# Performance work log

Measured on AMD Instinct MI355X. Metric: run time of the kernel, lower is better.

The kernel has to match this reference:

```python
import jax, jax.numpy as jnp
import numpy as np

N_QUBITS = 12
N_LAYERS = 6
BATCH = 512
DIM = 2 ** N_QUBITS


def _apply_1q(psi, G, wire):
    """Apply a single-qubit gate on `wire` (wire 0 = most significant).
    psi: [B, 2^n] complex. G: [2,2] (shared) or [B,2,2] (batched)."""
    B = psi.shape[0]
    left = 2 ** wire
    psi = psi.reshape(B, left, 2, -1)
    if G.ndim == 2:
        psi = jnp.einsum('ij,bxjy->bxiy', G, psi)
    else:
        psi = jnp.einsum('bij,bxjy->bxiy', G, psi)
    return psi.reshape(B, -1)


def _apply_cnot(psi, c, t):
    """CNOT with control c, target t on [B, 2^n] state."""
    B = psi.shape[0]
    ps = psi.reshape((B,) + (2,) * N_QUBITS)
    ca, ta = c + 1, t + 1
    c0 = jnp.take(ps, 0, axis=ca)
    c1 = jnp.take(ps, 1, axis=ca)
    flip_ax = ta if ta < ca else ta - 1
    c1 = jnp.flip(c1, axis=flip_ax)  # X on target within control=1 block
    ps = jnp.stack([c0, c1], axis=ca)
    return ps.reshape(B, -1)


def _circuit(x, weights):
    B = x.shape[0]
    psi = jnp.zeros((B, DIM), jnp.complex64).at[:, 0].set(1.0)

    # AngleEmbedding: RY(x_w) on each wire (batched gate matrices)
    h = 0.5 * x
    c, s = jnp.cos(h).astype(jnp.complex64), jnp.sin(h).astype(jnp.complex64)
    for w in range(N_QUBITS):
        G = jnp.stack([jnp.stack([c[:, w], -s[:, w]], -1),
                       jnp.stack([s[:, w], c[:, w]], -1)], -2)  # [B,2,2]
        psi = _apply_1q(psi, G, w)

    # StronglyEntanglingLayers: Rot(phi,theta,omega) per wire, then ring of CNOTs
    for l in range(N_LAYERS):
        phi, theta, omega = weights[l, :, 0], weights[l, :, 1], weights[l, :, 2]
        ct = jnp.cos(0.5 * theta).astype(jnp.complex64)
        st = jnp.sin(0.5 * theta).astype(jnp.complex64)
        ep = jnp.exp(-0.5j * (phi + omega).astype(jnp.complex64))
        em = jnp.exp(0.5j * (phi - omega).astype(jnp.complex64))
        # Rot = RZ(omega) RY(theta) RZ(phi)
        m00 = ep * ct
        m01 = -em * st
        m10 = jnp.conj(em) * st
        m11 = jnp.conj(ep) * ct
        for w in range(N_QUBITS):
            G = jnp.array([[m00[w], m01[w]], [m10[w], m11[w]]], jnp.complex64)
            psi = _apply_1q(psi, G, w)
        r = l % (N_QUBITS - 1) + 1
        for w in range(N_QUBITS):
            psi = _apply_cnot(psi, w, (w + r) % N_QUBITS)

    # <Z_w> for every wire
    probs = psi.real ** 2 + psi.imag ** 2  # [B, 2^n]
    exps = []
    for w in range(N_QUBITS):
        p = probs.reshape(B, 2 ** w, 2, -1)
        exps.append(p[:, :, 0, :].sum((1, 2)) - p[:, :, 1, :].sum((1, 2)))
    return jnp.stack(exps, -1)  # [B, n_qubits]


def setup_inputs() -> dict:
    key = jax.random.key(0)
    k1, k2, k3, k4 = jax.random.split(key, 4)
    x = jax.random.uniform(k1, (BATCH, N_QUBITS), jnp.float32, -np.pi, np.pi)
    weights = jax.random.uniform(k2, (N_LAYERS, N_QUBITS, 3), jnp.float32, 0.0, 2.0 * np.pi)
    W = jax.random.normal(k3, (1, N_QUBITS), jnp.float32) * 0.3
    b = jax.random.normal(k4, (1,), jnp.float32) * 0.01
    return {"x": x, "weights": weights, "W": W, "b": b}


def reference(x, weights, W, b):
    z = _circuit(x, weights)              # [B, n_qubits]
    y = z @ W.T + b                       # [B, 1]
    return y.squeeze(-1)                  # [B]
```

## Files before the change

kernel.cpp:

```cpp
#include <hip/hip_runtime.h>
#include <stdint.h>

#define NQ 12
#define DIM 4096
#define NLAYERS 6
#define TPB 256

typedef float v2f __attribute__((ext_vector_type(2)));

struct Pass_t {
    uint32_t WT[8];
    uint32_t WL[8];
    uint32_t RT[8];
    uint32_t RL[16];
    bool r64;
};
struct Pass10_t {
    uint32_t WT[6];
    uint32_t WL[8];
    uint32_t RT[6];
    uint32_t RL[16];
    bool r64;
};
struct CK_t {
    Pass10_t PS1, PS2;
    Pass_t PS3;
    Pass_t P1[NLAYERS];
    uint32_t frow[NQ];
};

constexpr uint32_t S1f(uint32_t k){ return ((k&7u)<<3) | ((k>>3)&7u) | (k & 0xFC0u); }
constexpr uint32_t S2f(uint32_t k){ return ((k&7u)<<6) | (k & 0x38u) | ((k>>6)&7u) | (k & 0xE00u); }
constexpr uint32_t S3f(uint32_t k){ return ((k&7u)<<9) | (k & 0x1F8u) | ((k>>9)&7u); }

constexpr uint32_t ech_reduce(const uint32_t* v, int n, uint32_t x){
    bool ch = true;
    while (ch) {
        ch = false;
        for (int i = 0; i < n; i++)
            if (v[i] && (x ^ v[i]) < x) { x ^= v[i]; ch = true; }
    }
    return x;
}

constexpr Pass_t build_pass(const uint32_t* Mc) {
    Pass_t P{};
    bool r64 = (Mc[3] == 8u);
    for (int j = 0; j < 12; j++) if (j != 3 && (Mc[j] & 8u)) r64 = false;
    P.r64 = r64;
    uint32_t rows[12]{};
    rows[0] = 8u;
    int nr = 1;
    uint32_t full[12]{}; int nf = 0; full[nf++] = 8u;
    uint32_t We[4]{};  int nw = 0;
    uint32_t Re[5]{};  int nre = 0;
    const int rpn = r64 ? 4 : 5;
    if (!r64) {
        uint32_t p0 = 0;
        for (int j = 0; j < rpn; j++)
            p0 |= (uint32_t)(__builtin_popcount(8u & Mc[4 + j]) & 1) << j;
        uint32_t r = ech_reduce(Re, nre, p0);
        if (r) Re[nre++] = r;
    }
    for (int slot = 0; slot < 4; slot++) {
        uint32_t chosen = 0;
        for (int relax = 0; relax < 3 && !chosen; relax++) {
            for (uint32_t m = 1; m < 4096u && !chosen; m++) {
                if (m & 8u) continue;
                uint32_t wp = (m >> 4) & 15u;
                uint32_t wr = ech_reduce(We, nw, wp);
                if (relax < 2 && !wr) continue;
                uint32_t rp = 0;
                for (int j = 0; j < rpn; j++)
                    rp |= (uint32_t)(__builtin_popcount(m & Mc[4 + j]) & 1) << j;
                uint32_t rr = ech_reduce(Re, nre, rp);
                if (relax < 1 && !rr) continue;
                uint32_t fr = ech_reduce(full, nf, m);
                if (!fr) continue;
                chosen = m; full[nf++] = fr;
                if (wr && nw < 4) We[nw++] = wr;
                if (rr && nre < 5) Re[nre++] = rr;
            }
        }
        rows[nr++] = chosen;
    }
    for (int slot = nr; slot < 12; slot++) {
        for (uint32_t m = 1; m < 4096u; m++) {
            if (m & 8u) continue;
            uint32_t fr = ech_reduce(full, nf, m);
            if (fr) { rows[slot] = m; full[nf++] = fr; break; }
        }
    }
    uint32_t col[12]{}, lmc[12]{};
    for (int j = 0; j < 12; j++) {
        uint32_t c = 0;
        for (int i = 0; i < 12; i++) c |= (uint32_t)((rows[i] >> j) & 1u) << i;
        col[j] = c;
    }
    for (int j = 0; j < 12; j++) {
        uint32_t a = 0, mc = Mc[j];
        for (int q = 0; q < 12; q++) if ((mc >> q) & 1u) a ^= col[q];
        lmc[j] = a;
    }
    for (int j = 0; j < 8; j++) { P.WT[j] = col[4 + j]; P.RT[j] = lmc[4 + j]; }
    for (int j = 0; j < 8; j++) {
        uint32_t a = 0;
        for (int q = 0; q < 3; q++) if ((j >> q) & 1) a ^= col[q];
        P.WL[j] = a;
    }
    for (int l = 0; l < 16; l++) {
        uint32_t a = 0;
        for (int q = 0; q < 4; q++) if ((l >> q) & 1) a ^= lmc[q];
        P.RL[l] = a;
    }
    return P;
}

constexpr Pass10_t build_pass10(const uint32_t* Mc) {
    Pass10_t P{};
    bool r64 = (Mc[3] == 8u);
    for (int j = 0; j < 10; j++) if (j != 3 && (Mc[j] & 8u)) r64 = false;
    P.r64 = r64;
    uint32_t rows[10]{};
    rows[0] = 8u;
    int nr = 1;
    uint32_t full[10]{}; int nf = 0; full[nf++] = 8u;
    uint32_t We[4]{};  int nw = 0;
    uint32_t Re[5]{};  int nre = 0;
    const int rpn = r64 ? 4 : 5;
    if (!r64) {
        uint32_t p0 = 0;
        for (int j = 0; j < rpn; j++)
            p0 |= (uint32_t)(__builtin_popcount(8u & Mc[4 + j]) & 1) << j;
        uint32_t r = ech_reduce(Re, nre, p0);
        if (r) Re[nre++] = r;
    }
    for (int slot = 0; slot < 4; slot++) {
        uint32_t chosen = 0;
        for (int relax = 0; relax < 3 && !chosen; relax++) {
            for (uint32_t m = 1; m < 1024u && !chosen; m++) {
                if (m & 8u) continue;
                uint32_t wp = (m >> 4) & 15u;
                uint32_t wr = ech_reduce(We, nw, wp);
                if (relax < 2 && !wr) continue;
                uint32_t rp = 0;
                for (int j = 0; j < rpn; j++)
                    rp |= (uint32_t)(__builtin_popcount(m & Mc[4 + j]) & 1) << j;
                uint32_t rr = ech_reduce(Re, nre, rp);
                if (relax < 1 && !rr) continue;
                uint32_t fr = ech_reduce(full, nf, m);
                if (!fr) continue;
                chosen = m; full[nf++] = fr;
                if (wr && nw < 4) We[nw++] = wr;
                if (rr && nre < 5) Re[nre++] = rr;
            }
        }
        rows[nr++] = chosen;
    }
    for (int slot = nr; slot < 10; slot++) {
        for (uint32_t m = 1; m < 1024u; m++) {
            if (m & 8u) continue;
            uint32_t fr = ech_reduce(full, nf, m);
            if (fr) { rows[slot] = m; full[nf++] = fr; break; }
        }
    }
    uint32_t col[10]{}, lmc[10]{};
    for (int j = 0; j < 10; j++) {
        uint32_t c = 0;
        for (int i = 0; i < 10; i++) c |= (uint32_t)((rows[i] >> j) & 1u) << i;
        col[j] = c;
    }
    for (int j = 0; j < 10; j++) {
        uint32_t a = 0, mc = Mc[j];
        for (int q = 0; q < 10; q++) if ((mc >> q) & 1u) a ^= col[q];
        lmc[j] = a;
    }
    for (int j = 0; j < 6; j++) { P.WT[j] = col[4 + j]; P.RT[j] = lmc[4 + j]; }
    for (int j = 0; j < 8; j++) {
        uint32_t a = 0;
        for (int q = 0; q < 3; q++) if ((j >> q) & 1) a ^= col[q];
        P.WL[j] = a;
    }
    for (int l = 0; l < 16; l++) {
        uint32_t a = 0;
        for (int q = 0; q < 4; q++) if ((l >> q) & 1) a ^= lmc[q];
        P.RL[l] = a;
    }
    return P;
}

constexpr CK_t build_ck() {
    CK_t ck{};
    uint32_t Acols[NLAYERS][NQ]{}, Aicol5[NQ]{};
    for (int l = 0; l < NLAYERS; l++) {
        int r = l % (NQ - 1) + 1;
        for (int q = 0; q < NQ; q++) {
            uint32_t v = 1u << q;
            for (int w = NQ - 1; w >= 0; w--) {
                int pc = NQ - 1 - w, pt = NQ - 1 - ((w + r) % NQ);
                v ^= ((v >> pc) & 1u) << pt;
            }
            Acols[l][q] = v;
            if (l == NLAYERS - 1) {
                uint32_t u = 1u << q;
                for (int w = 0; w < NQ; w++) {
                    int pc = NQ - 1 - w, pt = NQ - 1 - ((w + r) % NQ);
                    u ^= ((u >> pc) & 1u) << pt;
                }
                Aicol5[q] = u;
            }
        }
    }
    uint32_t Mc10[10]{};
    for (int j = 0; j < 10; j++) Mc10[j] = S1f(1u << j);
    ck.PS1 = build_pass10(Mc10);
    for (int j = 0; j < 10; j++) Mc10[j] = S2f(1u << j);
    ck.PS2 = build_pass10(Mc10);
    uint32_t Mc[12]{};
    for (int j = 0; j < 12; j++) Mc[j] = S3f(1u << j);
    ck.PS3 = build_pass(Mc);
    for (int l = 1; l < NLAYERS; l++) {
        for (int j = 0; j < 12; j++) Mc[j] = S3f(S2f(S1f(Acols[l - 1][j])));
        ck.P1[l] = build_pass(Mc);
    }
    uint32_t Mcol[NQ]{};
    for (int j = 0; j < NQ; j++) {
        uint32_t pj = S1f(S2f(S3f(1u << j)));
        uint32_t M = 0;
        for (int m = 0; m < NQ; m++) if ((pj >> m) & 1u) M ^= Aicol5[m];
        Mcol[j] = M;
    }
    for (int p = 0; p < NQ; p++) {
        uint32_t s = 0;
        for (int j = 0; j < NQ; j++) s |= ((Mcol[j] >> p) & 1u) << j;
        ck.frow[p] = s;
    }
    return ck;
}
constexpr CK_t CK = build_ck();
static_assert(CK.PS2.r64, "S2 must fix the pack bit (b64 reads)");
static_assert(CK.PS3.r64, "S3 must fix the pack bit (b64 reads)");

template<int Q>
__device__ __forceinline__ void gate_q(v2f (&PRE)[8], v2f (&PIM)[8], float4 m) {
    v2f bx = {m.x, m.x}, by = {m.y, m.y}, bz = {m.z, m.z}, bw = {m.w, m.w};
    #pragma unroll
    for (int j = 0; j < 8; j++) {
        if (j & (1 << Q)) continue;
        int j2 = j | (1 << Q);
        v2f re0 = PRE[j], im0 = PIM[j], re1 = PRE[j2], im1 = PIM[j2];
        PRE[j]  = __builtin_elementwise_fma(bx, re0,
                  __builtin_elementwise_fma(by, -im0,
                  __builtin_elementwise_fma(bz, re1, -bw * im1)));
        PIM[j]  = __builtin_elementwise_fma(bx, im0,
                  __builtin_elementwise_fma(by, re0,
                  __builtin_elementwise_fma(bz, im1, bw * re1)));
        PRE[j2] = __builtin_elementwise_fma(bx, re1,
                  __builtin_elementwise_fma(by, im1,
                  __builtin_elementwise_fma(bz, -re0, -bw * im0)));
        PIM[j2] = __builtin_elementwise_fma(bx, im1,
                  __builtin_elementwise_fma(by, -re1,
                  __builtin_elementwise_fma(bz, -im0, bw * re0)));
    }
}

__device__ __forceinline__ void gate3(v2f (&PRE)[8], v2f (&PIM)[8],
                                      float4 g0, float4 g1, float4 g2) {
    gate_q<0>(PRE, PIM, g0);
    gate_q<1>(PRE, PIM, g1);
    gate_q<2>(PRE, PIM, g2);
}

__device__ __forceinline__ void s1_pass(v2f (&PRE)[8], v2f (&PIM)[8],
                                        float* buf, uint32_t wb, uint32_t rb) {
    constexpr Pass10_t P = CK.PS1;
    v2f* bre = (v2f*)buf;
    v2f* bim = (v2f*)(buf + DIM);
    #pragma unroll
    for (int j = 0; j < 8; j++) {
        uint32_t s = (wb ^ P.WL[j]) >> 1;
        bre[s] = PRE[j]; bim[s] = PIM[j];
    }
    __asm__ volatile("s_waitcnt lgkmcnt(0)" ::: "memory");
    #pragma unroll
    for (int j = 0; j < 8; j++) {
        uint32_t s0 = rb ^ P.RL[j], s1 = rb ^ P.RL[j | 8];
        v2f re, im;
        re.x = buf[s0];       re.y = buf[s1];
        im.x = buf[DIM + s0]; im.y = buf[DIM + s1];
        PRE[j] = re; PIM[j] = im;
    }
}

__device__ __forceinline__ void s2_pass(v2f (&PRE)[8], v2f (&PIM)[8],
                                        float* buf, uint32_t wb, uint32_t rb) {
    constexpr Pass10_t P = CK.PS2;
    v2f* bre = (v2f*)buf;
    v2f* bim = (v2f*)(buf + DIM);
    #pragma unroll
    for (int j = 0; j < 8; j++) {
        uint32_t s = (wb ^ P.WL[j]) >> 1;
        bre[s] = PRE[j]; bim[s] = PIM[j];
    }
    __asm__ volatile("s_waitcnt lgkmcnt(0)" ::: "memory");
    #pragma unroll
    for (int j = 0; j < 8; j++) {
        uint32_t s = (rb ^ P.RL[j]) >> 1;
        PRE[j] = bre[s]; PIM[j] = bim[s];
    }
}

__device__ __forceinline__ void s3_pass(v2f (&PRE)[8], v2f (&PIM)[8],
                                        float* buf, uint32_t wb, uint32_t rb) {
    constexpr Pass_t P = CK.PS3;
    v2f* bre = (v2f*)buf;
    v2f* bim = (v2f*)(buf + DIM);
    __syncthreads();
    #pragma unroll
    for (int j = 0; j < 8; j++) {
        uint32_t s = (wb ^ P.WL[j]) >> 1;
        bre[s] = PRE[j]; bim[s] = PIM[j];
    }
    __syncthreads();
    #pragma unroll
    for (int j = 0; j < 8; j++) {
        uint32_t s = (rb ^ P.RL[j]) >> 1;
        PRE[j] = bre[s]; PIM[j] = bim[s];
    }
}

__device__ __forceinline__ void rebase_pass(v2f (&PRE)[8], v2f (&PIM)[8],
                                            float* buf, int tid, int l) {
    const Pass_t& P = CK.P1[l];
    uint32_t wb = 0, rb = 0;
    #pragma unroll
    for (int j = 0; j < 8; j++) {
        uint32_t sel = (uint32_t)(-(int)((tid >> j) & 1));
        wb ^= sel & P.WT[j];
        rb ^= sel & P.RT[j];
    }
    v2f* bre = (v2f*)buf;
    v2f* bim = (v2f*)(buf + DIM);
    #pragma unroll
    for (int j = 0; j < 8; j++) {
        uint32_t s = (wb ^ P.WL[j]) >> 1;
        bre[s] = PRE[j]; bim[s] = PIM[j];
    }
    __syncthreads();
    #pragma unroll
    for (int j = 0; j < 8; j++) {
        uint32_t s0 = rb ^ P.RL[j], s1 = rb ^ P.RL[j | 8];
        v2f re, im;
        re.x = buf[s0];       re.y = buf[s1];
        im.x = buf[DIM + s0]; im.y = buf[DIM + s1];
        PRE[j] = re; PIM[j] = im;
    }
}

__global__ __launch_bounds__(TPB) void qsim_kernel(
    const float* __restrict__ x,
    const float* __restrict__ weights,
    const float* __restrict__ Wp,
    const float* __restrict__ bptr,
    float* __restrict__ out)
{
    __shared__ float  lds[2 * 2 * DIM];
    __shared__ float4 smat[NLAYERS * NQ];
    __shared__ float  scs[NQ], sss[NQ];
    __shared__ float  red[4];

    const int tid = threadIdx.x;
    const int b   = blockIdx.x;

    if (tid < NQ) {
        float s_, c_;
        sincosf(0.5f * x[b * NQ + tid], &s_, &c_);
        scs[tid] = c_; sss[tid] = s_;
    }
    if (tid < NLAYERS * NQ) {
        float phi   = weights[tid * 3 + 0];
        float theta = weights[tid * 3 + 1];
        float omega = weights[tid * 3 + 2];
        float st, ct; sincosf(0.5f * theta, &st, &ct);
        float sp, cp; sincosf(0.5f * (phi + omega), &sp, &cp);
        float sm, cm; sincosf(0.5f * (phi - omega), &sm, &cm);
        smat[tid] = make_float4(cp * ct, -sp * ct, -cm * st, -sm * st);
    }
    __syncthreads();

    float base = 1.0f;
    #pragma unroll
    for (int j = 0; j < 8; j++) {
        int w = 7 - j;
        base *= ((tid >> j) & 1) ? sss[w] : scs[w];
    }
    v2f PRE[8], PIM[8];
    float c8 = scs[8], s8 = sss[8];
    #pragma unroll
    for (int j = 0; j < 8; j++) {
        float a = base;
        #pragma unroll
        for (int p = 0; p < 3; p++) {
            int w = NQ - 1 - p;
            a *= ((j >> p) & 1) ? sss[w] : scs[w];
        }
        PRE[j].x = a * c8;  PRE[j].y = a * s8;
        PIM[j].x = 0.0f;    PIM[j].y = 0.0f;
    }

    uint32_t s1wb = 0, s1rb = 0, s2wb = 0, s2rb = 0, s3wb = 0, s3rb = 0;
    {
        constexpr Pass10_t Q1 = CK.PS1;
        constexpr Pass10_t Q2 = CK.PS2;
        constexpr Pass_t   Q3 = CK.PS3;
        #pragma unroll
        for (int j = 0; j < 6; j++) {
            uint32_t sel = (uint32_t)(-(int)((tid >> j) & 1));
            s1wb ^= sel & Q1.WT[j]; s1rb ^= sel & Q1.RT[j];
            s2wb ^= sel & Q2.WT[j]; s2rb ^= sel & Q2.RT[j];
        }
        #pragma unroll
        for (int j = 0; j < 8; j++) {
            uint32_t sel = (uint32_t)(-(int)((tid >> j) & 1));
            s3wb ^= sel & Q3.WT[j]; s3rb ^= sel & Q3.RT[j];
        }
        uint32_t wvb = (uint32_t)(tid & 0xC0) << 4;
        s1wb |= wvb; s1rb |= wvb; s2wb |= wvb; s2rb |= wvb;
    }

    float* bufA = lds;
    float* bufB = lds + 2 * DIM;

    #pragma clang loop unroll(disable)
    for (int l = 0; l < NLAYERS; l++) {
        if (l > 0) rebase_pass(PRE, PIM, bufB, tid, l);
        const int sb = l * NQ;
        gate3(PRE, PIM, smat[sb + 11], smat[sb + 10], smat[sb + 9]);
        s1_pass(PRE, PIM, bufA, s1wb, s1rb);
        gate3(PRE, PIM, smat[sb + 8], smat[sb + 7], smat[sb + 6]);
        s2_pass(PRE, PIM, bufA, s2wb, s2rb);
        gate3(PRE, PIM, smat[sb + 5], smat[sb + 4], smat[sb + 3]);
        s3_pass(PRE, PIM, bufA, s3wb, s3rb);
        gate3(PRE, PIM, smat[sb + 2], smat[sb + 1], smat[sb + 0]);
    }

    const float bv = bptr[0];
    float wbT[NQ];
    #pragma unroll
    for (int p = 0; p < NQ; p++) {
        uint32_t row = CK.frow[p];
        int tp = __popc(tid & (int)(row >> 4)) & 1;
        float Wv = Wp[NQ - 1 - p];
        wbT[p] = tp ? -Wv : Wv;
    }
    v2f acc2 = {0.0f, 0.0f};
    #pragma unroll
    for (int j = 0; j < 8; j++) {
        float cx = bv, cy = bv;
        #pragma unroll
        for (int p = 0; p < NQ; p++) {
            uint32_t row = CK.frow[p];
            float s = (__popc(j & (int)(row & 7u)) & 1) ? -wbT[p] : wbT[p];
            cx += s;
            cy += (row & 8u) ? -s : s;
        }
        v2f c = {cx, cy};
        acc2 += (PRE[j] * PRE[j] + PIM[j] * PIM[j]) * c;
    }
    float acc = acc2.x + acc2.y;
    #pragma unroll
    for (int off = 32; off > 0; off >>= 1)
        acc += __shfl_down(acc, off, 64);
    if ((tid & 63) == 0) red[tid >> 6] = acc;
    __syncthreads();
    if (tid == 0) out[b] = red[0] + red[1] + red[2] + red[3];
}

extern "C" void kernel_launch(void* const* d_in, const int* in_sizes, int n_in,
                              void* d_out, int out_size, void* d_ws, size_t ws_size,
                              hipStream_t stream) {
    const float* x       = (const float*)d_in[0];
    const float* weights = (const float*)d_in[1];
    const float* W       = (const float*)d_in[2];
    const float* bptr    = (const float*)d_in[3];
    qsim_kernel<<<512, TPB, 0, stream>>>(x, weights, W, bptr, (float*)d_out);
}
```

Before: 91.86 us.

## Apply gates on packed lane qubit to cut LDS exchange passes per layer

Each thread's state is held as 8 v2f pairs, with the second float of each pair treated as a fourth local qubit. A new pack_gate applies a gate directly on that packed bit using a lane swap. Gates are now grouped four per stage, so only two LDS permutation passes (PA, PB) run per layer instead of three. The PB pass now reads scalar floats rather than b64 pairs, because its layout no longer keeps the pack bit fixed. This adds extra VALU swizzle work and non-vectorized LDS reads.

```diff
diff --git a/kernel.cpp b/kernel.cpp
--- a/kernel.cpp
+++ b/kernel.cpp
@@ -13,25 +13,22 @@
     uint32_t WL[8];
     uint32_t RT[8];
     uint32_t RL[16];
-    bool r64;
 };
 struct Pass10_t {
     uint32_t WT[6];
     uint32_t WL[8];
     uint32_t RT[6];
     uint32_t RL[16];
-    bool r64;
 };
 struct CK_t {
-    Pass10_t PS1, PS2;
-    Pass_t PS3;
+    Pass10_t PA;
+    Pass_t PB;
     Pass_t P1[NLAYERS];
     uint32_t frow[NQ];
 };
 
-constexpr uint32_t S1f(uint32_t k){ return ((k&7u)<<3) | ((k>>3)&7u) | (k & 0xFC0u); }
-constexpr uint32_t S2f(uint32_t k){ return ((k&7u)<<6) | (k & 0x38u) | ((k>>6)&7u) | (k & 0xE00u); }
-constexpr uint32_t S3f(uint32_t k){ return ((k&7u)<<9) | (k & 0x1F8u) | ((k>>9)&7u); }
+constexpr uint32_t G2f(uint32_t k){ return ((k&15u)<<8) | (k&0xF0u) | ((k>>8)&15u); }
+constexpr uint32_t G3f(uint32_t k){ return ((k&15u)<<4) | ((k>>4)&15u) | (k&0xF00u); }
 
 constexpr uint32_t ech_reduce(const uint32_t* v, int n, uint32_t x){
     bool ch = true;
@@ -45,19 +42,15 @@
 
 constexpr Pass_t build_pass(const uint32_t* Mc) {
     Pass_t P{};
-    bool r64 = (Mc[3] == 8u);
-    for (int j = 0; j < 12; j++) if (j != 3 && (Mc[j] & 8u)) r64 = false;
-    P.r64 = r64;
     uint32_t rows[12]{};
     rows[0] = 8u;
     int nr = 1;
     uint32_t full[12]{}; int nf = 0; full[nf++] = 8u;
     uint32_t We[4]{};  int nw = 0;
     uint32_t Re[5]{};  int nre = 0;
-    const int rpn = r64 ? 4 : 5;
-    if (!r64) {
+    {
         uint32_t p0 = 0;
-        for (int j = 0; j < rpn; j++)
+        for (int j = 0; j < 5; j++)
             p0 |= (uint32_t)(__builtin_popcount(8u & Mc[4 + j]) & 1) << j;
         uint32_t r = ech_reduce(Re, nre, p0);
         if (r) Re[nre++] = r;
@@ -71,7 +64,7 @@
                 uint32_t wr = ech_reduce(We, nw, wp);
                 if (relax < 2 && !wr) continue;
                 uint32_t rp = 0;
-                for (int j = 0; j < rpn; j++)
+                for (int j = 0; j < 5; j++)
                     rp |= (uint32_t)(__builtin_popcount(m & Mc[4 + j]) & 1) << j;
                 uint32_t rr = ech_reduce(Re, nre, rp);
                 if (relax < 1 && !rr) continue;
@@ -118,19 +111,15 @@
 
 constexpr Pass10_t build_pass10(const uint32_t* Mc) {
     Pass10_t P{};
-    bool r64 = (Mc[3] == 8u);
-    for (int j = 0; j < 10; j++) if (j != 3 && (Mc[j] & 8u)) r64 = false;
-    P.r64 = r64;
     uint32_t rows[10]{};
     rows[0] = 8u;
     int nr = 1;
     uint32_t full[10]{}; int nf = 0; full[nf++] = 8u;
     uint32_t We[4]{};  int nw = 0;
     uint32_t Re[5]{};  int nre = 0;
-    const int rpn = r64 ? 4 : 5;
-    if (!r64) {
+    {
         uint32_t p0 = 0;
-        for (int j = 0; j < rpn; j++)
+        for (int j = 0; j < 5; j++)
             p0 |= (uint32_t)(__builtin_popcount(8u & Mc[4 + j]) & 1) << j;
         uint32_t r = ech_reduce(Re, nre, p0);
         if (r) Re[nre++] = r;
@@ -144,7 +133,7 @@
                 uint32_t wr = ech_reduce(We, nw, wp);
                 if (relax < 2 && !wr) continue;
                 uint32_t rp = 0;
-                for (int j = 0; j < rpn; j++)
+                for (int j = 0; j < 5; j++)
                     rp |= (uint32_t)(__builtin_popcount(m & Mc[4 + j]) & 1) << j;
                 uint32_t rr = ech_reduce(Re, nre, rp);
                 if (relax < 1 && !rr) continue;
@@ -212,20 +201,18 @@
         }
     }
     uint32_t Mc10[10]{};
-    for (int j = 0; j < 10; j++) Mc10[j] = S1f(1u << j);
-    ck.PS1 = build_pass10(Mc10);
-    for (int j = 0; j < 10; j++) Mc10[j] = S2f(1u << j);
-    ck.PS2 = build_pass10(Mc10);
+    for (int j = 0; j < 10; j++) Mc10[j] = G3f(1u << j);
+    ck.PA = build_pass10(Mc10);
     uint32_t Mc[12]{};
-    for (int j = 0; j < 12; j++) Mc[j] = S3f(1u << j);
-    ck.PS3 = build_pass(Mc);
+    for (int j = 0; j < 12; j++) Mc[j] = G2f(1u << j);
+    ck.PB = build_pass(Mc);
     for (int l = 1; l < NLAYERS; l++) {
-        for (int j = 0; j < 12; j++) Mc[j] = S3f(S2f(S1f(Acols[l - 1][j])));
+        for (int j = 0; j < 12; j++) Mc[j] = G2f(G3f(Acols[l - 1][j]));
         ck.P1[l] = build_pass(Mc);
     }
     uint32_t Mcol[NQ]{};
     for (int j = 0; j < NQ; j++) {
-        uint32_t pj = S1f(S2f(S3f(1u << j)));
+        uint32_t pj = G3f(G2f(1u << j));
         uint32_t M = 0;
         for (int m = 0; m < NQ; m++) if ((pj >> m) & 1u) M ^= Aicol5[m];
         Mcol[j] = M;
@@ -238,8 +225,6 @@
     return ck;
 }
 constexpr CK_t CK = build_ck();
-static_assert(CK.PS2.r64, "S2 must fix the pack bit (b64 reads)");
-static_assert(CK.PS3.r64, "S3 must fix the pack bit (b64 reads)");
 
 template<int Q>
 __device__ __forceinline__ void gate_q(v2f (&PRE)[8], v2f (&PIM)[8], float4 m) {
@@ -264,16 +249,20 @@
     }
 }
 
-__device__ __forceinline__ void gate3(v2f (&PRE)[8], v2f (&PIM)[8],
-                                      float4 g0, float4 g1, float4 g2) {
-    gate_q<0>(PRE, PIM, g0);
-    gate_q<1>(PRE, PIM, g1);
-    gate_q<2>(PRE, PIM, g2);
-}
-
-__device__ __forceinline__ void s1_pass(v2f (&PRE)[8], v2f (&PIM)[8],
+__device__ __forceinline__ void pack_gate(v2f (&PRE)[8], v2f (&PIM)[8], float4 m) {
+    v2f d1 = {-m.y, m.y}, d2 = {m.z, -m.z};
+    #pragma unroll
+    for (int j = 0; j < 8; j++) {
+        v2f RE = PRE[j], IM = PIM[j];
+        v2f sR = {RE.y, RE.x}, sI = {IM.y, IM.x};
+        PRE[j] = m.x * RE + d1 * IM + d2 * sR - m.w * sI;
+        PIM[j] = m.x * IM - d1 * RE + d2 * sI + m.w * sR;
+    }
+}
+
+__device__ __forceinline__ void pa_pass(v2f (&PRE)[8], v2f (&PIM)[8],
                                         float* buf, uint32_t wb, uint32_t rb) {
-    constexpr Pass10_t P = CK.PS1;
+    constexpr Pass10_t P = CK.PA;
     v2f* bre = (v2f*)buf;
     v2f* bim = (v2f*)(buf + DIM);
     #pragma unroll
@@ -292,27 +281,9 @@
     }
 }
 
-__device__ __forceinline__ void s2_pass(v2f (&PRE)[8], v2f (&PIM)[8],
+__device__ __forceinline__ void pb_pass(v2f (&PRE)[8], v2f (&PIM)[8],
                                         float* buf, uint32_t wb, uint32_t rb) {
-    constexpr Pass10_t P = CK.PS2;
-    v2f* bre = (v2f*)buf;
-    v2f* bim = (v2f*)(buf + DIM);
-    #pragma unroll
-    for (int j = 0; j < 8; j++) {
-        uint32_t s = (wb ^ P.WL[j]) >> 1;
-        bre[s] = PRE[j]; bim[s] = PIM[j];
-    }
-    __asm__ volatile("s_waitcnt lgkmcnt(0)" ::: "memory");
-    #pragma unroll
-    for (int j = 0; j < 8; j++) {
-        uint32_t s = (rb ^ P.RL[j]) >> 1;
-        PRE[j] = bre[s]; PIM[j] = bim[s];
-    }
-}
-
-__device__ __forceinline__ void s3_pass(v2f (&PRE)[8], v2f (&PIM)[8],
-                                        float* buf, uint32_t wb, uint32_t rb) {
-    constexpr Pass_t P = CK.PS3;
+    constexpr Pass_t P = CK.PB;
     v2f* bre = (v2f*)buf;
     v2f* bim = (v2f*)(buf + DIM);
     __syncthreads();
@@ -324,8 +295,11 @@
     __syncthreads();
     #pragma unroll
     for (int j = 0; j < 8; j++) {
-        uint32_t s = (rb ^ P.RL[j]) >> 1;
-        PRE[j] = bre[s]; PIM[j] = bim[s];
+        uint32_t s0 = rb ^ P.RL[j], s1 = rb ^ P.RL[j | 8];
+        v2f re, im;
+        re.x = buf[s0];       re.y = buf[s1];
+        im.x = buf[DIM + s0]; im.y = buf[DIM + s1];
+        PRE[j] = re; PIM[j] = im;
     }
 }
 
@@ -408,24 +382,20 @@
         PIM[j].x = 0.0f;    PIM[j].y = 0.0f;
     }
 
-    uint32_t s1wb = 0, s1rb = 0, s2wb = 0, s2rb = 0, s3wb = 0, s3rb = 0;
+    uint32_t pawb = 0, parb = 0, pbwb = 0, pbrb = 0;
+    #pragma unroll
+    for (int j = 0; j < 6; j++) {
+        uint32_t sel = (uint32_t)(-(int)((tid >> j) & 1));
+        pawb ^= sel & CK.PA.WT[j]; parb ^= sel & CK.PA.RT[j];
+    }
+    #pragma unroll
+    for (int j = 0; j < 8; j++) {
+        uint32_t sel = (uint32_t)(-(int)((tid >> j) & 1));
+        pbwb ^= sel & CK.PB.WT[j]; pbrb ^= sel & CK.PB.RT[j];
+    }
     {
-        constexpr Pass10_t Q1 = CK.PS1;
-        constexpr Pass10_t Q2 = CK.PS2;
-        constexpr Pass_t   Q3 = CK.PS3;
-        #pragma unroll
-        for (int j = 0; j < 6; j++) {
-            uint32_t sel = (uint32_t)(-(int)((tid >> j) & 1));
-            s1wb ^= sel & Q1.WT[j]; s1rb ^= sel & Q1.RT[j];
-            s2wb ^= sel & Q2.WT[j]; s2rb ^= sel & Q2.RT[j];
-        }
-        #pragma unroll
-        for (int j = 0; j < 8; j++) {
-            uint32_t sel = (uint32_t)(-(int)((tid >> j) & 1));
-            s3wb ^= sel & Q3.WT[j]; s3rb ^= sel & Q3.RT[j];
-        }
         uint32_t wvb = (uint32_t)(tid & 0xC0) << 4;
-        s1wb |= wvb; s1rb |= wvb; s2wb |= wvb; s2rb |= wvb;
+        pawb |= wvb; parb |= wvb;
     }
 
     float* bufA = lds;
@@ -435,13 +405,20 @@
     for (int l = 0; l < NLAYERS; l++) {
         if (l > 0) rebase_pass(PRE, PIM, bufB, tid, l);
         const int sb = l * NQ;
-        gate3(PRE, PIM, smat[sb + 11], smat[sb + 10], smat[sb + 9]);
-        s1_pass(PRE, PIM, bufA, s1wb, s1rb);
-        gate3(PRE, PIM, smat[sb + 8], smat[sb + 7], smat[sb + 6]);
-        s2_pass(PRE, PIM, bufA, s2wb, s2rb);
-        gate3(PRE, PIM, smat[sb + 5], smat[sb + 4], smat[sb + 3]);
-        s3_pass(PRE, PIM, bufA, s3wb, s3rb);
-        gate3(PRE, PIM, smat[sb + 2], smat[sb + 1], smat[sb + 0]);
+        gate_q<0>(PRE, PIM, smat[sb + 11]);
+        gate_q<1>(PRE, PIM, smat[sb + 10]);
+        gate_q<2>(PRE, PIM, smat[sb + 9]);
+        pack_gate(PRE, PIM, smat[sb + 8]);
+        pa_pass(PRE, PIM, bufA, pawb, parb);
+        gate_q<0>(PRE, PIM, smat[sb + 7]);
+        gate_q<1>(PRE, PIM, smat[sb + 6]);
+        gate_q<2>(PRE, PIM, smat[sb + 5]);
+        pack_gate(PRE, PIM, smat[sb + 4]);
+        pb_pass(PRE, PIM, bufA, pbwb, pbrb);
+        gate_q<0>(PRE, PIM, smat[sb + 3]);
+        gate_q<1>(PRE, PIM, smat[sb + 2]);
+        gate_q<2>(PRE, PIM, smat[sb + 1]);
+        pack_gate(PRE, PIM, smat[sb + 0]);
     }
 
     const float bv = bptr[0];
```

Result: faster. 89.26 us (-2.8%).
